# Kernel tuning notes

Hardware: AMD Instinct MI355X
Metric: run time of the kernel (lower is better)

## Reference

```python
import jax, jax.numpy as jnp
import numpy as np

H = W = 256
C = 128
SCALE = 512 ** (-0.5)  # literal from the source, not 1/sqrt(C)


def _pool_mat(size, out):
    # adaptive_avg_pool1d matrix: row i averages input[start_i:end_i]
    i = np.arange(out)
    s = (i * size) // out
    e = ((i + 1) * size + out - 1) // out  # ceil
    P = np.zeros((out, size), np.float32)
    for k in range(out):
        P[k, s[k]:e[k]] = 1.0 / (e[k] - s[k])
    return jnp.asarray(P)


def adaptive_avg_pool2d(x, out):
    # x: [B, C, H, W] -> [B, C, out, out] via separable pooling matrices
    Ph = _pool_mat(x.shape[2], out)
    Pw = _pool_mat(x.shape[3], out)
    y = jnp.einsum('oh,bchw->bcow', Ph, x)
    return jnp.einsum('pw,bcow->bcop', Pw, y)


def setup_inputs() -> dict:
    key = jax.random.key(0)
    k1, k2 = jax.random.split(key)
    x5 = jax.random.normal(k1, (4, C, H, W), dtype=jnp.float32)
    W_out = jax.random.normal(k2, (C, C), dtype=jnp.float32) * 0.02
    b_out = jnp.zeros((C,), dtype=jnp.float32)
    return {"x5": x5, "W_out": W_out, "b_out": b_out}


def reference(x5, W_out, b_out):
    B = x5.shape[0]
    # Query: [B, N, C], N = H*W
    Query = x5.reshape(B, C, H * W).transpose(0, 2, 1)
    # multi-scale pooled keys
    p16 = adaptive_avg_pool2d(x5, 16)
    p12 = adaptive_avg_pool2d(x5, 12)
    p9 = adaptive_avg_pool2d(x5, 9)
    p7 = adaptive_avg_pool2d(x5, 7)
    p6 = adaptive_avg_pool2d(x5, 6)
    p3 = adaptive_avg_pool2d(x5, 3)
    p1 = adaptive_avg_pool2d(x5, 1)
    # Key: concat flattened pools in source order [3, 1, 9, 7, 16] -> [B, C, 396]
    Key = jnp.concatenate(
        [p.reshape(B, C, -1) for p in (p3, p1, p9, p7, p16)], axis=-1)
    Value = Key.transpose(0, 2, 1)  # [B, 396, C]
    # attention: [B, N, 396]
    attn = jax.nn.softmax(SCALE * jnp.einsum('bnc,bck->bnk', Query, Key), axis=-1)
    agg = jnp.einsum('bnk,bkc->bnc', attn, Value)  # [B, N, C]
    agg = agg.transpose(0, 2, 1).reshape(B, C, H, W)
    # 1x1 conv
    out = jnp.einsum('oc,bchw->bohw', W_out, agg) + b_out[None, :, None, None]
    return (out + x5, p12, p6)
```

## Files before the change

kernel.cpp:

```cpp
#include <hip/hip_runtime.h>
#include <hip/hip_bf16.h>

typedef short bf16x8 __attribute__((ext_vector_type(8)));
typedef float f32x4  __attribute__((ext_vector_type(4)));
typedef unsigned short u16;

#define B_N 4
#define C_N 128
#define HW_ 256
#define NPIX 65536
#define NK 396
#define NKP 400
#define OUT_MAIN ((size_t)B_N * C_N * NPIX)
#define P12_OFF OUT_MAIN
#define P6_OFF  (P12_OFF + (size_t)B_N * C_N * 144)

#define BUFSZ  32768
#define VT_OFF 16384
#define P_OFF  65536
#define LDS_BYTES 73728

static __device__ __forceinline__ u16 f2bf(float x) {
  __hip_bfloat16 h = __float2bfloat16(x);
  return *(u16*)&h;
}
static __device__ __forceinline__ unsigned pack2(float lo, float hi) {
  return ((unsigned)f2bf(hi) << 16) | f2bf(lo);
}
static __device__ __forceinline__ void gl_lds16(const void* g, void* l) {
  __builtin_amdgcn_global_load_lds(
      (const __attribute__((address_space(1))) unsigned*)g,
      (__attribute__((address_space(3))) unsigned*)l, 16, 0, 0);
}
#define MFMA32 __builtin_amdgcn_mfma_f32_16x16x32_bf16
#define LGKM0 do { asm volatile("s_waitcnt lgkmcnt(0)" ::: "memory"); \
                   __builtin_amdgcn_sched_barrier(0); } while (0)
#define BAR() do { __builtin_amdgcn_s_barrier(); \
                   __builtin_amdgcn_sched_barrier(0); } while (0)
#define VM8() do { asm volatile("s_waitcnt vmcnt(8)" ::: "memory"); \
                   __builtin_amdgcn_sched_barrier(0); } while (0)
#define VM3() do { asm volatile("s_waitcnt vmcnt(3)" ::: "memory"); \
                   __builtin_amdgcn_sched_barrier(0); } while (0)

__global__ __launch_bounds__(1024) void pool_kernel(
    const float* __restrict__ x5, const float* __restrict__ W_out,
    u16* __restrict__ wsK, u16* __restrict__ wsKT, u16* __restrict__ wsW,
    float* __restrict__ out)
{
  __shared__ float yh[54][257];
  const int tid = threadIdx.x;
  const int bc = blockIdx.x;
  const int b  = bc >> 7;
  const int c  = bc & 127;
  const float2* plane2 = (const float2*)(x5 + (size_t)bc * NPIX);
  const int w2 = tid & 127;
  const int q  = tid >> 7;
  const int h0 = q * 32;

  if (bc < 16) {
    const int idx = bc * 1024 + tid;
    wsW[idx] = f2bf(W_out[idx]);
  }

  for (int i = tid; i < 54 * 257; i += 1024) ((float*)yh)[i] = 0.f;
  __syncthreads();

  const int os_[7] = {16,12,9,7,6,3,1};
  const int ro_[7] = {0,16,28,37,44,50,53};
  float ax[7], ay[7], a2x[7], a2y[7], inv_[7];
  int r_[7], e_[7], s2_[7];
  #pragma unroll
  for (int s = 0; s < 7; ++s) {
    const int o = os_[s];
    const int r = (h0 * o) >> 8;
    const int sr = (r * 256) / o;
    r_[s]  = r;
    e_[s]  = ((r + 1) * 256 + o - 1) / o;
    s2_[s] = ((r + 1) * 256) / o;
    inv_[s] = 1.0f / (float)(e_[s] - sr);
    ax[s] = 0.f; ay[s] = 0.f; a2x[s] = 0.f; a2y[s] = 0.f;
  }

  #pragma unroll
  for (int g = 0; g < 4; ++g) {
    float2 vv[8];
    #pragma unroll
    for (int k = 0; k < 8; ++k) vv[k] = plane2[(h0 + g*8 + k) * 128 + w2];
    #pragma unroll
    for (int k = 0; k < 8; ++k) {
      const int h = h0 + g*8 + k;
      const float2 v = vv[k];
      #pragma unroll
      for (int s = 0; s < 7; ++s) {
        const int o = os_[s];
        ax[s] += v.x; ay[s] += v.y;
        if (h >= s2_[s]) { a2x[s] += v.x; a2y[s] += v.y; }
        if (h + 1 == e_[s]) {
          atomicAdd(&yh[ro_[s] + r_[s]][2*w2],     ax[s] * inv_[s]);
          atomicAdd(&yh[ro_[s] + r_[s]][2*w2 + 1], ay[s] * inv_[s]);
          r_[s]++;
          const int sr = s2_[s];
          e_[s]  = ((r_[s] + 1) * 256 + o - 1) / o;
          s2_[s] = ((r_[s] + 1) * 256) / o;
          inv_[s] = 1.0f / (float)(e_[s] - sr);
          ax[s] = a2x[s]; ay[s] = a2y[s];
          a2x[s] = 0.f; a2y[s] = 0.f;
        }
      }
    }
  }
  #pragma unroll
  for (int s = 0; s < 7; ++s) {
    const int o = os_[s];
    if (r_[s] < o) {
      atomicAdd(&yh[ro_[s] + r_[s]][2*w2],     ax[s] * inv_[s]);
      atomicAdd(&yh[ro_[s] + r_[s]][2*w2 + 1], ay[s] * inv_[s]);
      if (r_[s] + 1 < o && s2_[s] < h0 + 32) {
        const int sr2 = s2_[s];
        const int e2  = ((r_[s] + 2) * 256 + o - 1) / o;
        const float inv2 = 1.0f / (float)(e2 - sr2);
        atomicAdd(&yh[ro_[s] + r_[s] + 1][2*w2],     a2x[s] * inv2);
        atomicAdd(&yh[ro_[s] + r_[s] + 1][2*w2 + 1], a2y[s] * inv2);
      }
    }
  }
  __syncthreads();

  if (tid < NKP - NK) {
    wsK [((size_t)b * NKP + NK + tid) * C_N + c] = 0;
    wsKT[(size_t)bc * NKP + NK + tid] = 0;
  }

  const int grp = tid >> 4;
  const int gl  = tid & 15;
  #pragma unroll
  for (int it = 0; it < 9; ++it) {
    const int r = grp + it * 64;
    int rr = r;
    int o, ro, kbase, dst;
    if      (rr < 256) { o = 16; ro = 0;  kbase = 140; dst = 0; }
    else if (rr < 400) { o = 12; ro = 16; kbase = 0;   dst = 1; rr -= 256; }
    else if (rr < 481) { o = 9;  ro = 28; kbase = 10;  dst = 0; rr -= 400; }
    else if (rr < 530) { o = 7;  ro = 37; kbase = 91;  dst = 0; rr -= 481; }
    else if (rr < 566) { o = 6;  ro = 44; kbase = 0;   dst = 2; rr -= 530; }
    else if (rr < 575) { o = 3;  ro = 50; kbase = 0;   dst = 0; rr -= 566; }
    else               { o = 1;  ro = 53; kbase = 9;   dst = 0; rr = 0;   }
    const int i = rr / o;
    const int j = rr - i * o;
    const int s = (j * HW_) / o;
    const int e = ((j + 1) * HW_ + o - 1) / o;
    float partial = 0.f;
    const float* row = yh[ro + i];
    for (int wq = s + gl; wq < e; wq += 16) partial += row[wq];
    partial += __shfl_xor(partial, 1);
    partial += __shfl_xor(partial, 2);
    partial += __shfl_xor(partial, 4);
    partial += __shfl_xor(partial, 8);
    if (gl == 0) {
      const float v = partial * (1.0f / (float)(e - s));
      if (dst == 1) {
        out[P12_OFF + (size_t)bc * 144 + rr] = v;
      } else if (dst == 2) {
        out[P6_OFF + (size_t)bc * 36 + rr] = v;
      } else {
        const int key = kbase + rr;
        const u16 bv = f2bf(v);
        wsK [((size_t)b * NKP + key) * C_N + c] = bv;
        wsKT[(size_t)bc * NKP + key]            = bv;
      }
    }
  }
}

template<int CB, int BUF>
static __device__ __forceinline__ void stage64(
    char* smem, const char* wsKb, const char* wsKTb, int wv, int lane)
{
  char* buf = smem + BUF * BUFSZ;
  #pragma unroll
  for (int j = 0; j < 4; ++j) {
    const int krow = CB + j*16 + wv*4 + (lane >> 4);
    gl_lds16(wsKb + (size_t)krow * 256 + (((lane & 15) ^ (krow & 15)) << 4),
             buf + j*4096 + wv*1024);
    const int vrow = j*32 + wv*8 + (lane >> 3);
    gl_lds16(wsKTb + (size_t)vrow * (NKP*2) + CB*2 + (((lane & 7) ^ (vrow & 7)) << 4),
             buf + VT_OFF + j*4096 + wv*1024);
  }
}

static __device__ __forceinline__ void stage_tail(
    char* buf, const char* wsKb, const char* wsKTb, int wv, int lane)
{
  {
    const int row = wv*4 + (lane >> 4);
    gl_lds16(wsKb + (size_t)(384 + row) * 256 + (((lane & 15) ^ (row & 15)) << 4),
             buf + wv * 1024);
  }
  #pragma unroll
  for (int j = 0; j < 2; ++j) {
    const int row = j*64 + wv*16 + (lane >> 2);
    gl_lds16(wsKTb + (size_t)row * (NKP*2) + 768 + ((lane & 3) << 4),
             buf + VT_OFF + j*4096 + wv*1024);
  }
}

static __device__ __forceinline__ void stage_W(
    char* smem, const u16* wsW, int wv, int lane)
{
  #pragma unroll
  for (int j = 0; j < 8; ++j) {
    const int row = j*16 + wv*4 + (lane >> 4);
    gl_lds16((const char*)wsW + (size_t)row * 256 + (((lane & 15) ^ (row & 15)) << 4),
             smem + BUFSZ + j*4096 + wv*1024);
  }
}

template<int BUF, int TAIL>
static __device__ __forceinline__ void compute64(
    char* smem, char* pbase, const bf16x8 (&qf)[2][4],
    f32x4 (&agg)[8][2], float (&d)[2], int l15, int l4)
{
  const char* buf = smem + BUF * BUFSZ;
  constexpr int NT   = TAIL ? 1 : 4;
  constexpr int SUBS = TAIL ? 1 : 2;

  f32x4 sA[NT][2];
  #pragma unroll
  for (int nt = 0; nt < NT; ++nt) {
    sA[nt][0] = (f32x4){0.f,0.f,0.f,0.f};
    sA[nt][1] = (f32x4){0.f,0.f,0.f,0.f};
  }
  #pragma unroll
  for (int nt = 0; nt < NT; ++nt) {
    bf16x8 kf[4];
    #pragma unroll
    for (int kc = 0; kc < 4; ++kc)
      kf[kc] = *(const bf16x8*)(buf + (nt*16 + l15) * 256 +
                                ((kc*64 + l4*16) ^ (l15 << 4)));
    #pragma unroll
    for (int kc = 0; kc < 4; ++kc) {
      sA[nt][0] = MFMA32(kf[kc], qf[0][kc], sA[nt][0], 0, 0, 0);
      sA[nt][1] = MFMA32(kf[kc], qf[1][kc], sA[nt][1], 0, 0, 0);
    }
  }

  #pragma unroll
  for (int sub = 0; sub < SUBS; ++sub) {
    if (sub) LGKM0;
    #pragma unroll
    for (int pt = 0; pt < 2; ++pt) {
      const int prow = pt*16 + l15;
      const int sz2  = (prow & 3) << 4;
      #pragma unroll
      for (int u = 0; u < (TAIL ? 1 : 2); ++u) {
        const int nt = sub*2 + u;
        float p[4];
        #pragma unroll
        for (int qi = 0; qi < 4; ++qi) {
          float e = exp2f(sA[nt][pt][qi]);
          if (TAIL && (l4*4 + qi >= 12)) e = 0.f;
          p[qi] = e;
        }
        d[pt] += (p[0] + p[1]) + (p[2] + p[3]);
        uint2 pk;
        pk.x = pack2(p[0], p[1]);
        pk.y = pack2(p[2], p[3]);
        *(uint2*)(pbase + prow*64 + ((u*32 + l4*8) ^ sz2)) = pk;
      }
      if (TAIL) {
        uint2 z; z.x = 0u; z.y = 0u;
        *(uint2*)(pbase + prow*64 + ((32 + l4*8) ^ sz2)) = z;
      }
    }
    LGKM0;

    bf16x8 pf[2];
    #pragma unroll
    for (int pt = 0; pt < 2; ++pt) {
      const int prow = pt*16 + l15;
      pf[pt] = *(const bf16x8*)(pbase + prow*64 + ((l4*16) ^ ((prow & 3) << 4)));
    }
    #pragma unroll
    for (int ct = 0; ct < 8; ++ct) {
      const int vrow = ct*16 + l15;
      bf16x8 vf;
      if (TAIL)
        vf = *(const bf16x8*)(buf + VT_OFF + vrow*64 + l4*16);
      else
        vf = *(const bf16x8*)(buf + VT_OFF + vrow*128 +
                              ((sub*64 + l4*16) ^ ((vrow & 7) << 4)));
      agg[ct][0] = MFMA32(vf, pf[0], agg[ct][0], 0, 0, 0);
      agg[ct][1] = MFMA32(vf, pf[1], agg[ct][1], 0, 0, 0);
    }
  }
}

__global__ __launch_bounds__(256, 2) void attn_kernel(
    const float* __restrict__ x5, const u16* __restrict__ wsK,
    const u16* __restrict__ wsKT, const u16* __restrict__ wsW,
    const float* __restrict__ b_out, float* __restrict__ out)
{
  extern __shared__ char smem[];
  const int tid  = threadIdx.x;
  const int wgid = (blockIdx.x & 7) * 256 + (blockIdx.x >> 3);
  const int b    = wgid >> 9;
  const int pix0 = (wgid & 511) << 7;
  const int lane = tid & 63, wv = tid >> 6;
  const int l15  = lane & 15, l4 = lane >> 4;
  const float SCL2 = 0.044194173824159216f * 1.4426950408889634f;
  char* pbase = smem + P_OFF + wv * 2048;

  const char* wsKb  = (const char*)wsK  + (size_t)b * NKP * C_N * 2;
  const char* wsKTb = (const char*)wsKT + (size_t)b * C_N * NKP * 2;

  {
    const float* r0p = x5 + (((size_t)(b * C_N + 2*lane)) << 16) + pix0 + wv * 32;
    const float* r1p = r0p + NPIX;
    float4 v0[8], v1[8];
    #pragma unroll
    for (int j = 0; j < 8; ++j) {
      v0[j] = *(const float4*)(r0p + j*4);
      v1[j] = *(const float4*)(r1p + j*4);
    }
    #pragma unroll
    for (int i = 0; i < 32; ++i) {
      const int pix = wv * 32 + i;
      const unsigned pk = pack2(((const float*)&v0[i>>2])[i&3] * SCL2,
                                ((const float*)&v1[i>>2])[i&3] * SCL2);
      *(unsigned*)(smem + pix * 256 + ((lane*4) ^ ((pix & 15) << 4))) = pk;
    }
  }
  __syncthreads();

  bf16x8 qf[2][4];
  #pragma unroll
  for (int pt = 0; pt < 2; ++pt)
    #pragma unroll
    for (int kc = 0; kc < 4; ++kc)
      qf[pt][kc] = *(const bf16x8*)(smem + (wv*32 + pt*16 + l15) * 256 +
                                    ((kc*64 + l4*16) ^ (l15 << 4)));
  __syncthreads();

  f32x4 agg[8][2];
  #pragma unroll
  for (int ct = 0; ct < 8; ++ct) {
    agg[ct][0] = (f32x4){0.f,0.f,0.f,0.f};
    agg[ct][1] = (f32x4){0.f,0.f,0.f,0.f};
  }
  float d[2] = {0.f, 0.f};

  stage64<0, 0>(smem, wsKb, wsKTb, wv, lane);
  stage64<64, 1>(smem, wsKb, wsKTb, wv, lane);
  VM8(); BAR();
  compute64<0, 0>(smem, pbase, qf, agg, d, l15, l4);
  BAR();

  stage64<128, 0>(smem, wsKb, wsKTb, wv, lane);
  VM8(); BAR();
  compute64<1, 0>(smem, pbase, qf, agg, d, l15, l4);
  BAR();

  stage64<192, 1>(smem, wsKb, wsKTb, wv, lane);
  VM8(); BAR();
  compute64<0, 0>(smem, pbase, qf, agg, d, l15, l4);
  BAR();

  stage64<256, 0>(smem, wsKb, wsKTb, wv, lane);
  VM8(); BAR();
  compute64<1, 0>(smem, pbase, qf, agg, d, l15, l4);
  BAR();

  stage64<320, 1>(smem, wsKb, wsKTb, wv, lane);
  VM8(); BAR();
  compute64<0, 0>(smem, pbase, qf, agg, d, l15, l4);
  BAR();

  stage_tail(smem, wsKb, wsKTb, wv, lane);
  VM3(); BAR();
  compute64<1, 0>(smem, pbase, qf, agg, d, l15, l4);
  BAR();

  {
    f32x4 z = (f32x4){0.f,0.f,0.f,0.f};
    *(f32x4*)(smem + VT_OFF + (tid >> 1) * 64 + 32 + ((tid & 1) << 4)) = z;
  }
  stage_W(smem, wsW, wv, lane);
  asm volatile("s_waitcnt vmcnt(0)" ::: "memory");
  __syncthreads();

  compute64<0, 1>(smem, pbase, qf, agg, d, l15, l4);

  float inv[2];
  #pragma unroll
  for (int pt = 0; pt < 2; ++pt) {
    float s = d[pt];
    s += __shfl_xor(s, 16);
    s += __shfl_xor(s, 32);
    inv[pt] = 1.0f / s;
  }

  f32x4 cacc[8][2];
  #pragma unroll
  for (int ot = 0; ot < 8; ++ot) {
    cacc[ot][0] = (f32x4){0.f,0.f,0.f,0.f};
    cacc[ot][1] = (f32x4){0.f,0.f,0.f,0.f};
  }
  #pragma unroll
  for (int qh = 0; qh < 4; ++qh) {
    LGKM0;
    #pragma unroll
    for (int pt = 0; pt < 2; ++pt) {
      const int prow = pt*16 + l15;
      const int sz2  = (prow & 3) << 4;
      #pragma unroll
      for (int u = 0; u < 2; ++u) {
        const f32x4 a = agg[qh*2 + u][pt];
        uint2 pk;
        pk.x = pack2(a[0] * inv[pt], a[1] * inv[pt]);
        pk.y = pack2(a[2] * inv[pt], a[3] * inv[pt]);
        *(uint2*)(pbase + prow*64 + ((u*32 + l4*8) ^ sz2)) = pk;
      }
    }
    LGKM0;
    bf16x8 agf[2];
    #pragma unroll
    for (int pt = 0; pt < 2; ++pt) {
      const int prow = pt*16 + l15;
      agf[pt] = *(const bf16x8*)(pbase + prow*64 + ((l4*16) ^ ((prow & 3) << 4)));
    }
    #pragma unroll
    for (int ot = 0; ot < 8; ++ot) {
      const bf16x8 wa = *(const bf16x8*)(smem + BUFSZ + (ot*16 + l15) * 256 +
                                         ((qh*64 + l4*16) ^ (l15 << 4)));
      cacc[ot][0] = MFMA32(wa, agf[0], cacc[ot][0], 0, 0, 0);
      cacc[ot][1] = MFMA32(wa, agf[1], cacc[ot][1], 0, 0, 0);
    }
  }

  #pragma unroll
  for (int ot = 0; ot < 8; ++ot) {
    const float4 bq = *(const float4*)(b_out + ot*16 + l4*4);
    #pragma unroll
    for (int pt = 0; pt < 2; ++pt) {
      #pragma unroll
      for (int qi = 0; qi < 4; ++qi) {
        const int o = ot*16 + l4*4 + qi;
        const size_t idx = (((size_t)(b * C_N + o)) << 16) + pix0 + wv*32 + pt*16 + l15;
        out[idx] = cacc[ot][pt][qi] + ((const float*)&bq)[qi] + x5[idx];
      }
    }
  }
}

extern "C" void kernel_launch(void* const* d_in, const int* in_sizes, int n_in,
                              void* d_out, int out_size, void* d_ws, size_t ws_size,
                              hipStream_t stream) {
  const float* x5    = (const float*)d_in[0];
  const float* W_out = (const float*)d_in[1];
  const float* b_out = (const float*)d_in[2];
  float* out = (float*)d_out;
  u16* wsKT = (u16*)d_ws;
  u16* wsK  = (u16*)((char*)d_ws + (size_t)B_N * C_N * NKP * 2);
  u16* wsW  = (u16*)((char*)d_ws + (size_t)2 * B_N * C_N * NKP * 2);

  pool_kernel<<<512, 1024, 0, stream>>>(x5, W_out, wsK, wsKT, wsW, out);

  hipFuncSetAttribute((const void*)attn_kernel,
                      hipFuncAttributeMaxDynamicSharedMemorySize, LDS_BYTES);
  attn_kernel<<<B_N * 512, 256, LDS_BYTES, stream>>>(x5, wsK, wsKT, wsW, b_out, out);
}
```

Measured before the change: 205.0 us.

## Feed MFMA accumulators directly as operands via permuted K/W layouts, dropping LDS round-trip

Drops the per-wave LDS scratch buffer that held the softmax probabilities and the normalized aggregate before reloading them as MFMA B-operands. Instead, the key rows staged for QK^T and the W_out columns are permuted so each lane's accumulator values already sit in the right K positions for the next MFMA, and they are packed to bf16 in registers. This removes LDS writes, reads and lgkmcnt waits in the inner loop and lowers LDS use, at the cost of more complex index mapping. The tail step now handles two key tiles, and the pooling loop loads 16 rows per batch instead of 8.

```diff
diff --git a/kernel.cpp b/kernel.cpp
--- a/kernel.cpp
+++ b/kernel.cpp
@@ -17,8 +17,7 @@
 
 #define BUFSZ  32768
 #define VT_OFF 16384
-#define P_OFF  65536
-#define LDS_BYTES 73728
+#define LDS_BYTES 65536
 
 static __device__ __forceinline__ u16 f2bf(float x) {
   __hip_bfloat16 h = __float2bfloat16(x);
@@ -33,13 +32,11 @@
       (__attribute__((address_space(3))) unsigned*)l, 16, 0, 0);
 }
 #define MFMA32 __builtin_amdgcn_mfma_f32_16x16x32_bf16
-#define LGKM0 do { asm volatile("s_waitcnt lgkmcnt(0)" ::: "memory"); \
-                   __builtin_amdgcn_sched_barrier(0); } while (0)
 #define BAR() do { __builtin_amdgcn_s_barrier(); \
                    __builtin_amdgcn_sched_barrier(0); } while (0)
 #define VM8() do { asm volatile("s_waitcnt vmcnt(8)" ::: "memory"); \
                    __builtin_amdgcn_sched_barrier(0); } while (0)
-#define VM3() do { asm volatile("s_waitcnt vmcnt(3)" ::: "memory"); \
+#define VM4() do { asm volatile("s_waitcnt vmcnt(4)" ::: "memory"); \
                    __builtin_amdgcn_sched_barrier(0); } while (0)
 
 __global__ __launch_bounds__(1024) void pool_kernel(
@@ -59,7 +56,10 @@
 
   if (bc < 16) {
     const int idx = bc * 1024 + tid;
-    wsW[idx] = f2bf(W_out[idx]);
+    const int o = idx >> 7, pp = idx & 127;
+    const int q32 = pp >> 5, pos = pp & 31, g = pos >> 3, jj = pos & 7;
+    const int csrc = q32 * 32 + ((jj < 4) ? (g * 4 + jj) : (16 + g * 4 + (jj - 4)));
+    wsW[idx] = f2bf(W_out[o * 128 + csrc]);
   }
 
   for (int i = tid; i < 54 * 257; i += 1024) ((float*)yh)[i] = 0.f;
@@ -82,13 +82,13 @@
   }
 
   #pragma unroll
-  for (int g = 0; g < 4; ++g) {
-    float2 vv[8];
-    #pragma unroll
-    for (int k = 0; k < 8; ++k) vv[k] = plane2[(h0 + g*8 + k) * 128 + w2];
-    #pragma unroll
-    for (int k = 0; k < 8; ++k) {
-      const int h = h0 + g*8 + k;
+  for (int g = 0; g < 2; ++g) {
+    float2 vv[16];
+    #pragma unroll
+    for (int k = 0; k < 16; ++k) vv[k] = plane2[(h0 + g*16 + k) * 128 + w2];
+    #pragma unroll
+    for (int k = 0; k < 16; ++k) {
+      const int h = h0 + g*16 + k;
       const float2 v = vv[k];
       #pragma unroll
       for (int s = 0; s < 7; ++s) {
@@ -177,10 +177,12 @@
     char* smem, const char* wsKb, const char* wsKTb, int wv, int lane)
 {
   char* buf = smem + BUF * BUFSZ;
+  const int lr = lane >> 4, lc = lane & 15;
+  const int rit = wv * 4 + lr;
   #pragma unroll
   for (int j = 0; j < 4; ++j) {
-    const int krow = CB + j*16 + wv*4 + (lane >> 4);
-    gl_lds16(wsKb + (size_t)krow * 256 + (((lane & 15) ^ (krow & 15)) << 4),
+    const int gk = CB + (j >> 1) * 32 + wv * 8 + ((j & 1) << 2) + lr;
+    gl_lds16(wsKb + (size_t)gk * 256 + ((lc ^ rit) << 4),
              buf + j*4096 + wv*1024);
     const int vrow = j*32 + wv*8 + (lane >> 3);
     gl_lds16(wsKTb + (size_t)vrow * (NKP*2) + CB*2 + (((lane & 7) ^ (vrow & 7)) << 4),
@@ -191,10 +193,13 @@
 static __device__ __forceinline__ void stage_tail(
     char* buf, const char* wsKb, const char* wsKTb, int wv, int lane)
 {
-  {
-    const int row = wv*4 + (lane >> 4);
-    gl_lds16(wsKb + (size_t)(384 + row) * 256 + (((lane & 15) ^ (row & 15)) << 4),
-             buf + wv * 1024);
+  const int lr = lane >> 4;
+  const int rit = wv * 4 + lr;
+  #pragma unroll
+  for (int j = 0; j < 2; ++j) {
+    const int gk = 384 + wv * 8 + (j << 2) + lr;
+    gl_lds16(wsKb + (size_t)gk * 256 + (((lane & 15) ^ rit) << 4),
+             buf + j*4096 + wv*1024);
   }
   #pragma unroll
   for (int j = 0; j < 2; ++j) {
@@ -217,11 +222,11 @@
 
 template<int BUF, int TAIL>
 static __device__ __forceinline__ void compute64(
-    char* smem, char* pbase, const bf16x8 (&qf)[2][4],
+    char* smem, const bf16x8 (&qf)[2][4],
     f32x4 (&agg)[8][2], float (&d)[2], int l15, int l4)
 {
   const char* buf = smem + BUF * BUFSZ;
-  constexpr int NT   = TAIL ? 1 : 4;
+  constexpr int NT   = TAIL ? 2 : 4;
   constexpr int SUBS = TAIL ? 1 : 2;
 
   f32x4 sA[NT][2];
@@ -246,39 +251,23 @@
 
   #pragma unroll
   for (int sub = 0; sub < SUBS; ++sub) {
-    if (sub) LGKM0;
+    bf16x8 pf[2];
     #pragma unroll
     for (int pt = 0; pt < 2; ++pt) {
-      const int prow = pt*16 + l15;
-      const int sz2  = (prow & 3) << 4;
-      #pragma unroll
-      for (int u = 0; u < (TAIL ? 1 : 2); ++u) {
-        const int nt = sub*2 + u;
-        float p[4];
+      float e[8];
+      #pragma unroll
+      for (int qi = 0; qi < 4; ++qi) e[qi]     = exp2f(sA[2*sub][pt][qi]);
+      #pragma unroll
+      for (int qi = 0; qi < 4; ++qi) e[4 + qi] = exp2f(sA[2*sub + 1][pt][qi]);
+      if (TAIL) {
         #pragma unroll
-        for (int qi = 0; qi < 4; ++qi) {
-          float e = exp2f(sA[nt][pt][qi]);
-          if (TAIL && (l4*4 + qi >= 12)) e = 0.f;
-          p[qi] = e;
-        }
-        d[pt] += (p[0] + p[1]) + (p[2] + p[3]);
-        uint2 pk;
-        pk.x = pack2(p[0], p[1]);
-        pk.y = pack2(p[2], p[3]);
-        *(uint2*)(pbase + prow*64 + ((u*32 + l4*8) ^ sz2)) = pk;
+        for (int j = 0; j < 8; ++j) if (l4*8 + j >= 12) e[j] = 0.f;
       }
-      if (TAIL) {
-        uint2 z; z.x = 0u; z.y = 0u;
-        *(uint2*)(pbase + prow*64 + ((32 + l4*8) ^ sz2)) = z;
-      }
-    }
-    LGKM0;
-
-    bf16x8 pf[2];
-    #pragma unroll
-    for (int pt = 0; pt < 2; ++pt) {
-      const int prow = pt*16 + l15;
-      pf[pt] = *(const bf16x8*)(pbase + prow*64 + ((l4*16) ^ ((prow & 3) << 4)));
+      d[pt] += ((e[0]+e[1]) + (e[2]+e[3])) + ((e[4]+e[5]) + (e[6]+e[7]));
+      bf16x8 t;
+      #pragma unroll
+      for (int j = 0; j < 8; ++j) t[j] = (short)f2bf(e[j]);
+      pf[pt] = t;
     }
     #pragma unroll
     for (int ct = 0; ct < 8; ++ct) {
@@ -308,7 +297,6 @@
   const int lane = tid & 63, wv = tid >> 6;
   const int l15  = lane & 15, l4 = lane >> 4;
   const float SCL2 = 0.044194173824159216f * 1.4426950408889634f;
-  char* pbase = smem + P_OFF + wv * 2048;
 
   const char* wsKb  = (const char*)wsK  + (size_t)b * NKP * C_N * 2;
   const char* wsKTb = (const char*)wsKT + (size_t)b * C_N * NKP * 2;
@@ -352,43 +340,39 @@
   stage64<0, 0>(smem, wsKb, wsKTb, wv, lane);
   stage64<64, 1>(smem, wsKb, wsKTb, wv, lane);
   VM8(); BAR();
-  compute64<0, 0>(smem, pbase, qf, agg, d, l15, l4);
+  compute64<0, 0>(smem, qf, agg, d, l15, l4);
   BAR();
 
   stage64<128, 0>(smem, wsKb, wsKTb, wv, lane);
   VM8(); BAR();
-  compute64<1, 0>(smem, pbase, qf, agg, d, l15, l4);
+  compute64<1, 0>(smem, qf, agg, d, l15, l4);
   BAR();
 
   stage64<192, 1>(smem, wsKb, wsKTb, wv, lane);
   VM8(); BAR();
-  compute64<0, 0>(smem, pbase, qf, agg, d, l15, l4);
+  compute64<0, 0>(smem, qf, agg, d, l15, l4);
   BAR();
 
   stage64<256, 0>(smem, wsKb, wsKTb, wv, lane);
   VM8(); BAR();
-  compute64<1, 0>(smem, pbase, qf, agg, d, l15, l4);
+  compute64<1, 0>(smem, qf, agg, d, l15, l4);
   BAR();
 
   stage64<320, 1>(smem, wsKb, wsKTb, wv, lane);
   VM8(); BAR();
-  compute64<0, 0>(smem, pbase, qf, agg, d, l15, l4);
+  compute64<0, 0>(smem, qf, agg, d, l15, l4);
   BAR();
 
   stage_tail(smem, wsKb, wsKTb, wv, lane);
-  VM3(); BAR();
-  compute64<1, 0>(smem, pbase, qf, agg, d, l15, l4);
-  BAR();
-
-  {
-    f32x4 z = (f32x4){0.f,0.f,0.f,0.f};
-    *(f32x4*)(smem + VT_OFF + (tid >> 1) * 64 + 32 + ((tid & 1) << 4)) = z;
-  }
+  VM4(); BAR();
+  compute64<1, 0>(smem, qf, agg, d, l15, l4);
+  BAR();
+
   stage_W(smem, wsW, wv, lane);
   asm volatile("s_waitcnt vmcnt(0)" ::: "memory");
   __syncthreads();
 
-  compute64<0, 1>(smem, pbase, qf, agg, d, l15, l4);
+  compute64<0, 1>(smem, qf, agg, d, l15, l4);
 
   float inv[2];
   #pragma unroll
@@ -407,26 +391,14 @@
   }
   #pragma unroll
   for (int qh = 0; qh < 4; ++qh) {
-    LGKM0;
+    bf16x8 agf[2];
     #pragma unroll
     for (int pt = 0; pt < 2; ++pt) {
-      const int prow = pt*16 + l15;
-      const int sz2  = (prow & 3) << 4;
-      #pragma unroll
-      for (int u = 0; u < 2; ++u) {
-        const f32x4 a = agg[qh*2 + u][pt];
-        uint2 pk;
-        pk.x = pack2(a[0] * inv[pt], a[1] * inv[pt]);
-        pk.y = pack2(a[2] * inv[pt], a[3] * inv[pt]);
-        *(uint2*)(pbase + prow*64 + ((u*32 + l4*8) ^ sz2)) = pk;
-      }
-    }
-    LGKM0;
-    bf16x8 agf[2];
-    #pragma unroll
-    for (int pt = 0; pt < 2; ++pt) {
-      const int prow = pt*16 + l15;
-      agf[pt] = *(const bf16x8*)(pbase + prow*64 + ((l4*16) ^ ((prow & 3) << 4)));
+      bf16x8 t;
+      #pragma unroll
+      for (int j = 0; j < 8; ++j)
+        t[j] = (short)f2bf(agg[2*qh + (j >> 2)][pt][j & 3] * inv[pt]);
+      agf[pt] = t;
     }
     #pragma unroll
     for (int ot = 0; ot < 8; ++ot) {
```

Result: faster. 195.9 us (-4.5%).
